# Performance work log

Measured on AMD Instinct MI355X. Metric: run time of the kernel, lower is better.

Reference implementation:

```python
import jax, jax.numpy as jnp
import numpy as np

UNITS = 1024
D_Q = 1024
D_V = 1024


def setup_inputs() -> dict:
    key = jax.random.key(0)
    ks = jax.random.split(key, 8)
    B, S = 32, 2048
    query = jax.random.normal(ks[0], (B, D_Q), dtype=jnp.float32)
    values = jax.random.normal(ks[1], (B, S, D_V), dtype=jnp.float32)
    # Keras Dense params (glorot-ish scale for weights, zero bias init kept random-free)
    W1 = jax.random.normal(ks[2], (D_V, UNITS), dtype=jnp.float32) / np.sqrt(D_V)
    b1 = jnp.zeros((UNITS,), dtype=jnp.float32)
    W2 = jax.random.normal(ks[3], (D_Q, UNITS), dtype=jnp.float32) / np.sqrt(D_Q)
    b2 = jnp.zeros((UNITS,), dtype=jnp.float32)
    V = jax.random.normal(ks[4], (UNITS, 1), dtype=jnp.float32) / np.sqrt(UNITS)
    bV = jnp.zeros((1,), dtype=jnp.float32)
    return {"query": query, "values": values, "W1": W1, "b1": b1,
            "W2": W2, "b2": b2, "V": V, "bV": bV}


def reference(query, values, W1, b1, W2, b2, V, bV):
    # query: [B, d_q], values: [B, S, d_v]
    proj_v = jnp.einsum('bsd,du->bsu', values, W1) + b1        # [B, S, U]
    proj_q = (query @ W2 + b2)[:, None, :]                      # [B, 1, U]
    score = jnp.tanh(proj_v + proj_q) @ V + bV                  # [B, S, 1]
    attention_weights = jax.nn.softmax(score, axis=1)           # [B, S, 1]
    context_vector = jnp.sum(attention_weights * values, axis=1)  # [B, d_v]
    return (context_vector, attention_weights)
```

## Files before the change

kernel.cpp:

```cpp
#include <hip/hip_runtime.h>
#include <math.h>

#define B_  32
#define S_  2048
#define DV  1024
#define U_  1024

typedef __attribute__((ext_vector_type(8))) short bf16x8;
typedef __attribute__((ext_vector_type(4))) float f32x4;

__device__ inline unsigned short f2bf(float f) {
    unsigned int x = __float_as_uint(f);
    return (unsigned short)((x + 0x7fffu + ((x >> 16) & 1u)) >> 16);
}

__device__ inline uint4 pack8(float4 a, float4 b) {
    union { unsigned short s[8]; uint4 u; } p;
    p.s[0] = f2bf(a.x); p.s[1] = f2bf(a.y); p.s[2] = f2bf(a.z); p.s[3] = f2bf(a.w);
    p.s[4] = f2bf(b.x); p.s[5] = f2bf(b.y); p.s[6] = f2bf(b.z); p.s[7] = f2bf(b.w);
    return p.u;
}

__device__ inline float tanh_fast(float x) {
    float ax = fabsf(x);
    float e  = __expf(ax + ax);
    float t  = 1.0f - __fdividef(2.0f, e + 1.0f);
    return copysignf(t, x);
}

__device__ __forceinline__ void gload16(const void* g, void* l) {
    __builtin_amdgcn_global_load_lds(
        (const __attribute__((address_space(1))) void*)g,
        (__attribute__((address_space(3))) void*)l,
        16, 0, 0);
}

#define ASM_VMCNT(N) asm volatile("s_waitcnt vmcnt(" #N ")" ::: "memory")
#define ASM_LGKM0()  do { asm volatile("s_waitcnt lgkmcnt(0)" ::: "memory"); \
                          __builtin_amdgcn_sched_barrier(0); } while (0)

__global__ __launch_bounds__(256)
void prep_small(const float* __restrict__ W1, unsigned short* __restrict__ W1T,
                const float* __restrict__ query, const float* __restrict__ W2,
                const float* __restrict__ b1, const float* __restrict__ b2,
                float* __restrict__ t, float* __restrict__ scores) {
    const int bid = blockIdx.x;
    const int tid = threadIdx.x;

    if (bid < 256) {
        __shared__ float tile[64][65];
        int k0 = (bid & 15) * 64, u0 = (bid >> 4) * 64;
        int lr = tid >> 4, lc = (tid & 15) * 4;
#pragma unroll
        for (int j = 0; j < 4; ++j) {
            float4 f = *(const float4*)&W1[(size_t)(k0 + lr + j * 16) * U_ + u0 + lc];
            tile[lr + j * 16][lc + 0] = f.x; tile[lr + j * 16][lc + 1] = f.y;
            tile[lr + j * 16][lc + 2] = f.z; tile[lr + j * 16][lc + 3] = f.w;
        }
        __syncthreads();
        int ur = tid >> 2, kq = (tid & 3) * 16;
        union { unsigned short s[8]; uint4 u; } p0, p1;
#pragma unroll
        for (int e = 0; e < 8; ++e) p0.s[e] = f2bf(tile[kq + e][ur]);
#pragma unroll
        for (int e = 0; e < 8; ++e) p1.s[e] = f2bf(tile[kq + 8 + e][ur]);
        unsigned short* dst = W1T + (size_t)(u0 + ur) * 1024 + k0 + kq;
        *(uint4*)dst       = p0.u;
        *(uint4*)(dst + 8) = p1.u;
    } else if (bid < 384) {
        __shared__ float qs2[1024];
        int i = bid - 256;
        int b = i >> 2, uq = i & 3;
        for (int j = tid; j < 1024; j += 256) qs2[j] = query[b * DV + j];
        __syncthreads();
        int u = uq * 256 + tid;
        float a0 = 0.f, a1 = 0.f, a2 = 0.f, a3 = 0.f;
        float a4 = 0.f, a5 = 0.f, a6 = 0.f, a7 = 0.f;
        const float* w = W2 + u;
        for (int k = 0; k < 1024; k += 8) {
            a0 += qs2[k + 0] * w[(size_t)(k + 0) * U_];
            a1 += qs2[k + 1] * w[(size_t)(k + 1) * U_];
            a2 += qs2[k + 2] * w[(size_t)(k + 2) * U_];
            a3 += qs2[k + 3] * w[(size_t)(k + 3) * U_];
            a4 += qs2[k + 4] * w[(size_t)(k + 4) * U_];
            a5 += qs2[k + 5] * w[(size_t)(k + 5) * U_];
            a6 += qs2[k + 6] * w[(size_t)(k + 6) * U_];
            a7 += qs2[k + 7] * w[(size_t)(k + 7) * U_];
        }
        t[b * U_ + u] = b1[u] + b2[u]
                      + ((a0 + a1) + (a2 + a3)) + ((a4 + a5) + (a6 + a7));
    } else {
        scores[(bid - 384) * 256 + tid] = 0.f;
    }
}

__global__ __launch_bounds__(256)
void cvt_lines(const float* __restrict__ v, char* __restrict__ o) {
    const int bid   = blockIdx.x;
    const int stile = bid >> 4;
    const int kt    = bid & 15;
    const int tid   = threadIdx.x;
    const int h     = tid >> 7;
    const int r     = tid & 127;
    const int row   = stile * 256 + h * 128 + r;
    const float4* src = (const float4*)(v + (size_t)row * 1024 + kt * 64);
    float4 f[16];
#pragma unroll
    for (int j = 0; j < 16; ++j) f[j] = src[j];
    char* dst = o + (size_t)stile * 524288 + kt * 32768 + h * 16384 + r * 128;
    const int rx = r & 7;
#pragma unroll
    for (int c = 0; c < 8; ++c) {
        uint4 w = pack8(f[2 * c], f[2 * c + 1]);
        *(uint4*)(dst + ((c ^ rx) << 4)) = w;
    }
}

#define MFMA16(MB, NB)                                                          \
    _Pragma("unroll") for (int ks = 0; ks < 2; ++ks)                            \
    _Pragma("unroll") for (int n = 0; n < 2; ++n)                               \
    _Pragma("unroll") for (int m = 0; m < 4; ++m)                               \
        acc[(MB)+m][(NB)+n] = __builtin_amdgcn_mfma_f32_16x16x32_bf16(          \
            af[m][ks], bf[n][ks], acc[(MB)+m][(NB)+n], 0, 0, 0);

__launch_bounds__(512, 2)
__global__ void scores_mfma8(const char* __restrict__ AbfT,
                             const unsigned short* __restrict__ W1T,
                             const float* __restrict__ tvec,
                             const float* __restrict__ V,
                             float* __restrict__ scores) {
    __shared__ __align__(16) char lds[131072];

    const int tid  = threadIdx.x;
    const int lane = tid & 63;
    const int wave = tid >> 6;
    const int wm   = wave >> 2;
    const int wn   = wave & 3;
    const int l15  = lane & 15;
    const int lq   = lane >> 4;

    const int id    = blockIdx.x;
    const int wg    = (id & 7) * 128 + (id >> 3);
    const int utile = wg & 3;
    const int stile = wg >> 2;
    const size_t row0 = (size_t)stile * 256;
    const int b       = (int)(row0 >> 11);
    const int s_local = (int)(row0 & 2047);
    const int u0      = utile * 256;

    const char* aBase = AbfT + (size_t)stile * 524288 + wave * 1024 + lane * 16;
    const int rowst = wave * 8 + (lane >> 3);
    const int kch8  = ((lane & 7) ^ ((lane >> 3) & 7)) * 8;
    const unsigned short* bSrc = W1T + (size_t)(u0 + rowst) * 1024 + kch8;
    char* const dstW = lds + wave * 1024;

    const int ao0 = wm * 16384 + l15 * 128 + ((lq ^ (l15 & 7)) << 4);
    const int ao1 = ao0 ^ 64;
    const int bo0 = 32768 + (wn >> 1) * 16384 + (wn & 1) * 8192
                  + l15 * 128 + ((lq ^ (l15 & 7)) << 4);
    const int bo1 = bo0 ^ 64;

    f32x4 acc[8][4];
#pragma unroll
    for (int m = 0; m < 8; ++m)
#pragma unroll
        for (int n = 0; n < 4; ++n) acc[m][n] = (f32x4)0.f;

    bf16x8 af[4][2];
    bf16x8 bf[2][2];

    auto stageA = [&](size_t gOff, int dOff) {
        gload16(aBase + gOff,        dstW + dOff);
        gload16(aBase + gOff + 8192, dstW + dOff + 8192);
    };
    auto stageB = [&](const unsigned short* s, int dOff) {
        gload16(s,             dstW + dOff);
        gload16(s + 64 * 1024, dstW + dOff + 8192);
    };
    auto readA4 = [&](int base) {
#pragma unroll
        for (int m = 0; m < 4; ++m) {
            af[m][0] = *(const bf16x8*)(lds + base + m * 2048 + ao0);
            af[m][1] = *(const bf16x8*)(lds + base + m * 2048 + ao1);
        }
    };
    auto readB2 = [&](int base) {
#pragma unroll
        for (int n = 0; n < 2; ++n) {
            bf[n][0] = *(const bf16x8*)(lds + base + n * 2048 + bo0);
            bf[n][1] = *(const bf16x8*)(lds + base + n * 2048 + bo1);
        }
    };

    stageA(0,     0);
    stageA(16384, 16384);
    stageB(bSrc,          32768);
    stageB(bSrc + 131072, 49152);
    stageA(32768, 65536);
    __builtin_amdgcn_sched_barrier(0);
    ASM_VMCNT(2);
    __builtin_amdgcn_s_barrier();
    __builtin_amdgcn_sched_barrier(0);

    for (int it = 0; it < 8; ++it) {
        const bool pf = (it < 7);
        const size_t aIt = (size_t)it * 65536;
        readA4(0);
        readB2(0);
        stageA(aIt + 49152, 81920);
        __builtin_amdgcn_s_barrier();
        ASM_LGKM0();
        __builtin_amdgcn_s_setprio(1);
        MFMA16(0, 0);
        __builtin_amdgcn_s_setprio(0);
        __builtin_amdgcn_s_barrier();
        readB2(2 * 2048);
        stageB(bSrc + 64, 98304);
        __builtin_amdgcn_s_barrier();
        ASM_LGKM0();
        __builtin_amdgcn_s_setprio(1);
        MFMA16(0, 2);
        __builtin_amdgcn_s_setprio(0);
        __builtin_amdgcn_s_barrier();
        readA4(4 * 2048);
        stageB(bSrc + 64 + 131072, 114688);
        __builtin_amdgcn_s_barrier();
        ASM_LGKM0();
        __builtin_amdgcn_s_setprio(1);
        MFMA16(4, 2);
        __builtin_amdgcn_s_setprio(0);
        __builtin_amdgcn_s_barrier();
        readB2(0);
        if (pf) stageA(aIt + 65536, 0);
        __builtin_amdgcn_s_barrier();
        ASM_LGKM0();
        __builtin_amdgcn_s_setprio(1);
        MFMA16(4, 0);
        __builtin_amdgcn_s_setprio(0);
        __builtin_amdgcn_sched_barrier(0);
        if (pf) { ASM_VMCNT(2); } else { ASM_VMCNT(0); }
        __builtin_amdgcn_s_barrier();
        __builtin_amdgcn_sched_barrier(0);
        readA4(65536);
        readB2(65536);
        if (pf) stageA(aIt + 81920, 16384);
        __builtin_amdgcn_s_barrier();
        ASM_LGKM0();
        __builtin_amdgcn_s_setprio(1);
        MFMA16(0, 0);
        __builtin_amdgcn_s_setprio(0);
        __builtin_amdgcn_s_barrier();
        readB2(65536 + 2 * 2048);
        if (pf) stageB(bSrc + 128, 32768);
        __builtin_amdgcn_s_barrier();
        ASM_LGKM0();
        __builtin_amdgcn_s_setprio(1);
        MFMA16(0, 2);
        __builtin_amdgcn_s_setprio(0);
        __builtin_amdgcn_s_barrier();
        if (pf) stageB(bSrc + 128 + 131072, 49152);
        readA4(65536 + 4 * 2048);
        __builtin_amdgcn_s_barrier();
        ASM_LGKM0();
        __builtin_amdgcn_s_setprio(1);
        MFMA16(4, 2);
        __builtin_amdgcn_s_setprio(0);
        __builtin_amdgcn_s_barrier();
        readB2(65536);
        if (pf) stageA(aIt + 98304, 65536);
        __builtin_amdgcn_s_barrier();
        ASM_LGKM0();
        __builtin_amdgcn_s_setprio(1);
        MFMA16(4, 0);
        __builtin_amdgcn_s_setprio(0);
        __builtin_amdgcn_sched_barrier(0);
        if (pf) { ASM_VMCNT(2); }
        __builtin_amdgcn_s_barrier();
        __builtin_amdgcn_sched_barrier(0);

        bSrc += 128;
    }

    __syncthreads();
    float* fscore = (float*)lds;
    if (tid < 256) fscore[tid] = 0.f;
    __syncthreads();
    float tu[4], vu[4];
#pragma unroll
    for (int n = 0; n < 4; ++n) {
        int u = u0 + wn * 64 + n * 16 + l15;
        tu[n] = tvec[b * U_ + u];
        vu[n] = V[u];
    }
#pragma unroll
    for (int m = 0; m < 8; ++m) {
#pragma unroll
        for (int r = 0; r < 4; ++r) {
            float p = 0.f;
#pragma unroll
            for (int n = 0; n < 4; ++n) p += tanh_fast(acc[m][n][r] + tu[n]) * vu[n];
            p += __shfl_xor(p, 1);
            p += __shfl_xor(p, 2);
            p += __shfl_xor(p, 4);
            p += __shfl_xor(p, 8);
            if (l15 == 0) atomicAdd(&fscore[wm * 128 + m * 16 + lq * 4 + r], p);
        }
    }
    __syncthreads();
    if (tid < 256) atomicAdd(&scores[(size_t)b * S_ + s_local + tid], fscore[tid]);
}

__global__ __launch_bounds__(256)
void sm_ctx_part(const float* __restrict__ scores, const float* __restrict__ values,
                 float* __restrict__ wout, float* __restrict__ ctxp) {
    const int b   = blockIdx.x;
    const int sc  = blockIdx.y;
    const int tid = threadIdx.x;
    __shared__ float red[256];
    __shared__ float ws_[128];

    float v[8];
    float m = -1e30f;
#pragma unroll
    for (int i = 0; i < 8; ++i) {
        v[i] = scores[(size_t)b * S_ + tid + i * 256];
        m = fmaxf(m, v[i]);
    }
    red[tid] = m; __syncthreads();
    for (int off = 128; off > 0; off >>= 1) {
        if (tid < off) red[tid] = fmaxf(red[tid], red[tid + off]);
        __syncthreads();
    }
    m = red[0];
    __syncthreads();
    float s = 0.f;
#pragma unroll
    for (int i = 0; i < 8; ++i) s += __expf(v[i] - m);
    red[tid] = s; __syncthreads();
    for (int off = 128; off > 0; off >>= 1) {
        if (tid < off) red[tid] += red[tid + off];
        __syncthreads();
    }
    float inv = 1.f / red[0];
    __syncthreads();

    if (tid < 128) {
        float x = scores[(size_t)b * S_ + sc * 128 + tid];
        float w = __expf(x - m) * inv;
        ws_[tid] = w;
        wout[(size_t)b * S_ + sc * 128 + tid] = w;
    }
    __syncthreads();

    const float4* vp = (const float4*)(values + ((size_t)b * S_ + sc * 128) * DV) + tid;
    float ax = 0.f, ay = 0.f, az = 0.f, aw = 0.f;
#pragma unroll 4
    for (int s2 = 0; s2 < 128; ++s2) {
        float4 vv = vp[(size_t)s2 * 256];
        float wv = ws_[s2];
        ax += wv * vv.x; ay += wv * vv.y; az += wv * vv.z; aw += wv * vv.w;
    }
    float4 outv; outv.x = ax; outv.y = ay; outv.z = az; outv.w = aw;
    *(float4*)(ctxp + ((size_t)(b * 16 + sc)) * 1024 + tid * 4) = outv;
}

__global__ __launch_bounds__(256)
void ctx_reduce(const float* __restrict__ ctxp, float* __restrict__ ctx) {
    const int b  = blockIdx.x;
    const int dq = blockIdx.y;
    const int d  = dq * 256 + threadIdx.x;
    const float* p = ctxp + (size_t)b * 16 * 1024 + d;
    float s = 0.f;
#pragma unroll
    for (int sc = 0; sc < 16; ++sc) s += p[sc * 1024];
    ctx[b * DV + d] = s;
}

__global__ void init_kernel(const float* __restrict__ b1, const float* __restrict__ b2,
                            float* __restrict__ t, float* __restrict__ ctx,
                            float* __restrict__ scores) {
    int i = blockIdx.x * 256 + threadIdx.x;
    scores[i] = 0.f;
    if (i < B_ * U_) {
        int u = i & (U_ - 1);
        t[i]   = b1[u] + b2[u];
        ctx[i] = 0.f;
    }
}

__global__ void projq_kernel(const float* __restrict__ q, const float* __restrict__ W2,
                             float* __restrict__ t) {
    int b  = blockIdx.x;
    int ks = blockIdx.y;
    int tid = threadIdx.x;
    __shared__ float qs[64];
    if (tid < 64) qs[tid] = q[b * DV + ks * 64 + tid];
    __syncthreads();
    float a0 = 0.f, a1 = 0.f, a2 = 0.f, a3 = 0.f;
    const float* w = W2 + (size_t)(ks * 64) * U_;
    for (int d = 0; d < 64; ++d) {
        float qd = qs[d];
        const float* wr = w + (size_t)d * U_ + tid;
        a0 += qd * wr[0];
        a1 += qd * wr[256];
        a2 += qd * wr[512];
        a3 += qd * wr[768];
    }
    atomicAdd(&t[b * U_ + tid      ], a0);
    atomicAdd(&t[b * U_ + tid + 256], a1);
    atomicAdd(&t[b * U_ + tid + 512], a2);
    atomicAdd(&t[b * U_ + tid + 768], a3);
}

__launch_bounds__(256, 2)
__global__ void scores_vec(const float* __restrict__ values, const float* __restrict__ W1,
                           const float* __restrict__ t, const float* __restrict__ V,
                           float* __restrict__ scores) {
    __shared__ float vA[16][132];
    __shared__ float vB[16][68];
    __shared__ float fscore[128];
    const int b   = blockIdx.y;
    const int s0  = blockIdx.x * 128;
    const int tid = threadIdx.x;
    const int tx  = tid & 15, ty = tid >> 4;
    if (tid < 128) fscore[tid] = 0.f;
    const float* vbase = values + ((size_t)b * S_ + s0) * (size_t)DV;
    const int lm = tid >> 2, lkq = (tid & 3) * 4;
    const int lbk = tid >> 4, lbj = (tid & 15) * 4;
    for (int nt = 0; nt < U_ / 64; ++nt) {
        const int u0 = nt * 64;
        float acc[8][4];
#pragma unroll
        for (int i = 0; i < 8; ++i)
#pragma unroll
            for (int j = 0; j < 4; ++j) acc[i][j] = 0.f;
        for (int k0 = 0; k0 < DV; k0 += 16) {
            __syncthreads();
            const float4 v0 = *(const float4*)(vbase + (size_t)lm * DV + k0 + lkq);
            const float4 v1 = *(const float4*)(vbase + (size_t)(lm + 64) * DV + k0 + lkq);
            vA[lkq + 0][lm] = v0.x; vA[lkq + 1][lm] = v0.y;
            vA[lkq + 2][lm] = v0.z; vA[lkq + 3][lm] = v0.w;
            vA[lkq + 0][lm + 64] = v1.x; vA[lkq + 1][lm + 64] = v1.y;
            vA[lkq + 2][lm + 64] = v1.z; vA[lkq + 3][lm + 64] = v1.w;
            *(float4*)&vB[lbk][lbj] = *(const float4*)(W1 + (size_t)(k0 + lbk) * U_ + u0 + lbj);
            __syncthreads();
#pragma unroll
            for (int k = 0; k < 16; ++k) {
                float4 va0 = *(const float4*)&vA[k][ty * 8];
                float4 va1 = *(const float4*)&vA[k][ty * 8 + 4];
                float4 vb  = *(const float4*)&vB[k][tx * 4];
                float a_[8] = {va0.x, va0.y, va0.z, va0.w, va1.x, va1.y, va1.z, va1.w};
                float b_[4] = {vb.x, vb.y, vb.z, vb.w};
#pragma unroll
                for (int i = 0; i < 8; ++i)
#pragma unroll
                    for (int j = 0; j < 4; ++j) acc[i][j] += a_[i] * b_[j];
            }
        }
        float tq[4], vv[4];
#pragma unroll
        for (int j = 0; j < 4; ++j) {
            int u = u0 + tx * 4 + j;
            tq[j] = t[b * U_ + u];
            vv[j] = V[u];
        }
#pragma unroll
        for (int i = 0; i < 8; ++i) {
            float p = 0.f;
#pragma unroll
            for (int j = 0; j < 4; ++j) p += tanhf(acc[i][j] + tq[j]) * vv[j];
            p += __shfl_down(p, 8, 16);
            p += __shfl_down(p, 4, 16);
            p += __shfl_down(p, 2, 16);
            p += __shfl_down(p, 1, 16);
            if (tx == 0) fscore[ty * 8 + i] += p;
        }
    }
    __syncthreads();
    if (tid < 128) scores[(size_t)b * S_ + s0 + tid] = fscore[tid];
}

__global__ void softmax_kernel(const float* __restrict__ scores, float* __restrict__ wout) {
    int b = blockIdx.x;
    int tid = threadIdx.x;
    __shared__ float red[256];
    float v[8];
    float m = -1e30f;
#pragma unroll
    for (int i = 0; i < 8; ++i) {
        v[i] = scores[(size_t)b * S_ + tid + i * 256];
        m = fmaxf(m, v[i]);
    }
    red[tid] = m; __syncthreads();
    for (int off = 128; off > 0; off >>= 1) {
        if (tid < off) red[tid] = fmaxf(red[tid], red[tid + off]);
        __syncthreads();
    }
    m = red[0];
    __syncthreads();
    float s = 0.f;
#pragma unroll
    for (int i = 0; i < 8; ++i) { v[i] = __expf(v[i] - m); s += v[i]; }
    red[tid] = s; __syncthreads();
    for (int off = 128; off > 0; off >>= 1) {
        if (tid < off) red[tid] += red[tid + off];
        __syncthreads();
    }
    float inv = 1.f / red[0];
#pragma unroll
    for (int i = 0; i < 8; ++i) wout[(size_t)b * S_ + tid + i * 256] = v[i] * inv;
}

__global__ void context_kernel(const float* __restrict__ values, const float* __restrict__ w,
                               float* __restrict__ ctx) {
    int b   = blockIdx.x;
    int sc  = blockIdx.y;
    int tid = threadIdx.x;
    __shared__ float ws_[128];
    if (tid < 128) ws_[tid] = w[(size_t)b * S_ + sc * 128 + tid];
    __syncthreads();
    const float4* vp = (const float4*)(values + ((size_t)b * S_ + sc * 128) * DV) + tid;
    float ax = 0.f, ay = 0.f, az = 0.f, aw = 0.f;
#pragma unroll 4
    for (int s = 0; s < 128; ++s) {
        float4 v = vp[(size_t)s * 256];
        float wv = ws_[s];
        ax += wv * v.x; ay += wv * v.y; az += wv * v.z; aw += wv * v.w;
    }
    float* c = ctx + b * DV + tid * 4;
    atomicAdd(c + 0, ax); atomicAdd(c + 1, ay);
    atomicAdd(c + 2, az); atomicAdd(c + 3, aw);
}

extern "C" void kernel_launch(void* const* d_in, const int* in_sizes, int n_in,
                              void* d_out, int out_size, void* d_ws, size_t ws_size,
                              hipStream_t stream) {
    const float* query  = (const float*)d_in[0];
    const float* values = (const float*)d_in[1];
    const float* W1     = (const float*)d_in[2];
    const float* b1     = (const float*)d_in[3];
    const float* W2     = (const float*)d_in[4];
    const float* b2     = (const float*)d_in[5];
    const float* V      = (const float*)d_in[6];

    float* out  = (float*)d_out;
    float* ctx  = out;
    float* wout = out + B_ * DV;

    char* ws = (char*)d_ws;
    const size_t W1T_BYTES  = (size_t)U_ * DV * 2;
    const size_t T_BYTES    = (size_t)B_ * U_ * 4;
    const size_t SC_BYTES   = (size_t)B_ * S_ * 4;
    const size_t CTXP_BYTES = (size_t)B_ * 16 * DV * 4;
    const size_t ABF_BYTES  = (size_t)B_ * S_ * DV * 2;

    if (ws_size >= W1T_BYTES + T_BYTES + SC_BYTES + CTXP_BYTES + ABF_BYTES) {
        unsigned short* W1T = (unsigned short*)ws;
        float* t      = (float*)(ws + W1T_BYTES);
        float* scores = t + B_ * U_;
        float* ctxp   = scores + B_ * S_;
        char*  AbfT   = (char*)(ctxp + B_ * 16 * DV);

        prep_small  <<<dim3(640),    256, 0, stream>>>(W1, W1T, query, W2,
                                                       b1, b2, t, scores);
        cvt_lines   <<<dim3(4096),   256, 0, stream>>>(values, AbfT);
        scores_mfma8<<<dim3(1024),   512, 0, stream>>>(AbfT, W1T, t, V, scores);
        sm_ctx_part <<<dim3(32, 16), 256, 0, stream>>>(scores, values, wout, ctxp);
        ctx_reduce  <<<dim3(32, 4),  256, 0, stream>>>(ctxp, ctx);
    } else {
        float* t      = (float*)ws;
        float* scores = t + B_ * U_;

        init_kernel   <<<dim3(256),      256, 0, stream>>>(b1, b2, t, ctx, scores);
        projq_kernel  <<<dim3(32, 16),   256, 0, stream>>>(query, W2, t);
        scores_vec    <<<dim3(16, 32),   256, 0, stream>>>(values, W1, t, V, scores);
        softmax_kernel<<<dim3(32),       256, 0, stream>>>(scores, wout);
        context_kernel<<<dim3(32, 16),   256, 0, stream>>>(values, wout, ctx);
    }
}
```

Before: 674.6 us.

## Fuse fp32-to-bf16 conversion of values into the MFMA score kernel

Removes the separate cvt_lines pass that wrote a bf16, swizzled copy of values to workspace. The MFMA kernel now loads fp32 values straight into registers, converts them to bf16 and writes them to LDS inside its software pipeline, using register-staged prefetch with adjusted vmcnt waits. This avoids one full read and write of the 256MB values tensor plus the extra bf16 reread. The cost is more register pressure, fp32 global reads that are twice the size of the old bf16 reads, and VALU conversion work inside the MFMA loop, with stricter vmcnt(0) syncs.

```diff
diff --git a/kernel.cpp b/kernel.cpp
--- a/kernel.cpp
+++ b/kernel.cpp
@@ -94,28 +94,6 @@
     }
 }
 
-__global__ __launch_bounds__(256)
-void cvt_lines(const float* __restrict__ v, char* __restrict__ o) {
-    const int bid   = blockIdx.x;
-    const int stile = bid >> 4;
-    const int kt    = bid & 15;
-    const int tid   = threadIdx.x;
-    const int h     = tid >> 7;
-    const int r     = tid & 127;
-    const int row   = stile * 256 + h * 128 + r;
-    const float4* src = (const float4*)(v + (size_t)row * 1024 + kt * 64);
-    float4 f[16];
-#pragma unroll
-    for (int j = 0; j < 16; ++j) f[j] = src[j];
-    char* dst = o + (size_t)stile * 524288 + kt * 32768 + h * 16384 + r * 128;
-    const int rx = r & 7;
-#pragma unroll
-    for (int c = 0; c < 8; ++c) {
-        uint4 w = pack8(f[2 * c], f[2 * c + 1]);
-        *(uint4*)(dst + ((c ^ rx) << 4)) = w;
-    }
-}
-
 #define MFMA16(MB, NB)                                                          \
     _Pragma("unroll") for (int ks = 0; ks < 2; ++ks)                            \
     _Pragma("unroll") for (int n = 0; n < 2; ++n)                               \
@@ -123,12 +101,20 @@
         acc[(MB)+m][(NB)+n] = __builtin_amdgcn_mfma_f32_16x16x32_bf16(          \
             af[m][ks], bf[n][ks], acc[(MB)+m][(NB)+n], 0, 0, 0);
 
+#define ISSUEA(Sa, Sb, Sc, Sd, kt, h) do {                                      \
+    const float4* _s = (const float4*)(aRow + (size_t)(h) * 131072 + (kt) * 64);\
+    Sa = _s[0]; Sb = _s[1]; Sc = _s[2]; Sd = _s[3]; } while (0)
+
+#define WRITEA(Sa, Sb, Sc, Sd, dOff) do {                                       \
+    *(uint4*)(lds + (dOff) + wO0) = pack8(Sa, Sb);                              \
+    *(uint4*)(lds + (dOff) + wO1) = pack8(Sc, Sd); } while (0)
+
 __launch_bounds__(512, 2)
-__global__ void scores_mfma8(const char* __restrict__ AbfT,
-                             const unsigned short* __restrict__ W1T,
-                             const float* __restrict__ tvec,
-                             const float* __restrict__ V,
-                             float* __restrict__ scores) {
+__global__ void scores_mfma8g(const float* __restrict__ values,
+                              const unsigned short* __restrict__ W1T,
+                              const float* __restrict__ tvec,
+                              const float* __restrict__ V,
+                              float* __restrict__ scores) {
     __shared__ __align__(16) char lds[131072];
 
     const int tid  = threadIdx.x;
@@ -148,11 +134,17 @@
     const int s_local = (int)(row0 & 2047);
     const int u0      = utile * 256;
 
-    const char* aBase = AbfT + (size_t)stile * 524288 + wave * 1024 + lane * 16;
     const int rowst = wave * 8 + (lane >> 3);
     const int kch8  = ((lane & 7) ^ ((lane >> 3) & 7)) * 8;
     const unsigned short* bSrc = W1T + (size_t)(u0 + rowst) * 1024 + kch8;
     char* const dstW = lds + wave * 1024;
+
+    const int rA  = tid >> 2;
+    const int kcA = tid & 3;
+    const int c0  = (2 * kcA) ^ (rA & 7);
+    const int wO0 = rA * 128 + c0 * 16;
+    const int wO1 = rA * 128 + (c0 ^ 1) * 16;
+    const float* aRow = values + (row0 + rA) * 1024 + kcA * 16;
 
     const int ao0 = wm * 16384 + l15 * 128 + ((lq ^ (l15 & 7)) << 4);
     const int ao1 = ao0 ^ 64;
@@ -169,10 +161,6 @@
     bf16x8 af[4][2];
     bf16x8 bf[2][2];
 
-    auto stageA = [&](size_t gOff, int dOff) {
-        gload16(aBase + gOff,        dstW + dOff);
-        gload16(aBase + gOff + 8192, dstW + dOff + 8192);
-    };
     auto stageB = [&](const unsigned short* s, int dOff) {
         gload16(s,             dstW + dOff);
         gload16(s + 64 * 1024, dstW + dOff + 8192);
@@ -192,22 +180,31 @@
         }
     };
 
-    stageA(0,     0);
-    stageA(16384, 16384);
+    float4 Pa, Pb, Pc, Pd;
+    float4 Qa, Qb, Qc, Qd;
+    float4 Ra, Rb, Rc, Rd;
+    float4 Sa, Sb, Sc, Sd;
+
+    ISSUEA(Pa, Pb, Pc, Pd, 0, 0); ASM_VMCNT(0); WRITEA(Pa, Pb, Pc, Pd, 0);
+    ISSUEA(Pa, Pb, Pc, Pd, 0, 1); ASM_VMCNT(0); WRITEA(Pa, Pb, Pc, Pd, 16384);
+    ISSUEA(Pa, Pb, Pc, Pd, 1, 0); ASM_VMCNT(0); WRITEA(Pa, Pb, Pc, Pd, 65536);
     stageB(bSrc,          32768);
     stageB(bSrc + 131072, 49152);
-    stageA(32768, 65536);
-    __builtin_amdgcn_sched_barrier(0);
-    ASM_VMCNT(2);
+    ISSUEA(Pa, Pb, Pc, Pd, 1, 1);
+    ASM_VMCNT(0);
+    ASM_LGKM0();
     __builtin_amdgcn_s_barrier();
     __builtin_amdgcn_sched_barrier(0);
 
     for (int it = 0; it < 8; ++it) {
         const bool pf = (it < 7);
-        const size_t aIt = (size_t)it * 65536;
+        WRITEA(Pa, Pb, Pc, Pd, 81920);
         readA4(0);
         readB2(0);
-        stageA(aIt + 49152, 81920);
+        if (pf) {
+            ISSUEA(Qa, Qb, Qc, Qd, 2 * it + 2, 0);
+            ISSUEA(Ra, Rb, Rc, Rd, 2 * it + 2, 1);
+        }
         __builtin_amdgcn_s_barrier();
         ASM_LGKM0();
         __builtin_amdgcn_s_setprio(1);
@@ -231,19 +228,26 @@
         __builtin_amdgcn_s_setprio(0);
         __builtin_amdgcn_s_barrier();
         readB2(0);
-        if (pf) stageA(aIt + 65536, 0);
+        if (pf) {
+            ASM_VMCNT(8);
+            WRITEA(Qa, Qb, Qc, Qd, 0);
+        }
         __builtin_amdgcn_s_barrier();
         ASM_LGKM0();
         __builtin_amdgcn_s_setprio(1);
         MFMA16(4, 0);
         __builtin_amdgcn_s_setprio(0);
         __builtin_amdgcn_sched_barrier(0);
-        if (pf) { ASM_VMCNT(2); } else { ASM_VMCNT(0); }
+        ASM_VMCNT(0);
         __builtin_amdgcn_s_barrier();
         __builtin_amdgcn_sched_barrier(0);
+        if (pf) WRITEA(Ra, Rb, Rc, Rd, 16384);
         readA4(65536);
         readB2(65536);
-        if (pf) stageA(aIt + 81920, 16384);
+        if (pf) {
+            ISSUEA(Sa, Sb, Sc, Sd, 2 * it + 3, 0);
+            ISSUEA(Pa, Pb, Pc, Pd, 2 * it + 3, 1);
+        }
         __builtin_amdgcn_s_barrier();
         ASM_LGKM0();
         __builtin_amdgcn_s_setprio(1);
@@ -258,8 +262,8 @@
         MFMA16(0, 2);
         __builtin_amdgcn_s_setprio(0);
         __builtin_amdgcn_s_barrier();
+        readA4(65536 + 4 * 2048);
         if (pf) stageB(bSrc + 128 + 131072, 49152);
-        readA4(65536 + 4 * 2048);
         __builtin_amdgcn_s_barrier();
         ASM_LGKM0();
         __builtin_amdgcn_s_setprio(1);
@@ -267,14 +271,17 @@
         __builtin_amdgcn_s_setprio(0);
         __builtin_amdgcn_s_barrier();
         readB2(65536);
-        if (pf) stageA(aIt + 98304, 65536);
+        if (pf) {
+            ASM_VMCNT(8);
+            WRITEA(Sa, Sb, Sc, Sd, 65536);
+        }
         __builtin_amdgcn_s_barrier();
         ASM_LGKM0();
         __builtin_amdgcn_s_setprio(1);
         MFMA16(4, 0);
         __builtin_amdgcn_s_setprio(0);
         __builtin_amdgcn_sched_barrier(0);
-        if (pf) { ASM_VMCNT(2); }
+        ASM_VMCNT(0);
         __builtin_amdgcn_s_barrier();
         __builtin_amdgcn_sched_barrier(0);
 
@@ -552,21 +559,18 @@
     const size_t T_BYTES    = (size_t)B_ * U_ * 4;
     const size_t SC_BYTES   = (size_t)B_ * S_ * 4;
     const size_t CTXP_BYTES = (size_t)B_ * 16 * DV * 4;
-    const size_t ABF_BYTES  = (size_t)B_ * S_ * DV * 2;
-
-    if (ws_size >= W1T_BYTES + T_BYTES + SC_BYTES + CTXP_BYTES + ABF_BYTES) {
+
+    if (ws_size >= W1T_BYTES + T_BYTES + SC_BYTES + CTXP_BYTES) {
         unsigned short* W1T = (unsigned short*)ws;
         float* t      = (float*)(ws + W1T_BYTES);
         float* scores = t + B_ * U_;
         float* ctxp   = scores + B_ * S_;
-        char*  AbfT   = (char*)(ctxp + B_ * 16 * DV);
-
-        prep_small  <<<dim3(640),    256, 0, stream>>>(W1, W1T, query, W2,
-                                                       b1, b2, t, scores);
-        cvt_lines   <<<dim3(4096),   256, 0, stream>>>(values, AbfT);
-        scores_mfma8<<<dim3(1024),   512, 0, stream>>>(AbfT, W1T, t, V, scores);
-        sm_ctx_part <<<dim3(32, 16), 256, 0, stream>>>(scores, values, wout, ctxp);
-        ctx_reduce  <<<dim3(32, 4),  256, 0, stream>>>(ctxp, ctx);
+
+        prep_small   <<<dim3(640),    256, 0, stream>>>(W1, W1T, query, W2,
+                                                        b1, b2, t, scores);
+        scores_mfma8g<<<dim3(1024),   512, 0, stream>>>(values, W1T, t, V, scores);
+        sm_ctx_part  <<<dim3(32, 16), 256, 0, stream>>>(scores, values, wout, ctxp);
+        ctx_reduce   <<<dim3(32, 4),  256, 0, stream>>>(ctxp, ctx);
     } else {
         float* t      = (float*)ws;
         float* scores = t + B_ * U_;
```

After: 646.7 us. -4.1%, faster.
